# Kernel tuning notes

Hardware: AMD Instinct MI355X
Metric: run time of the kernel (lower is better)

The kernel has to match this reference:

```python
import jax, jax.numpy as jnp
import numpy as np
from jax import lax

SR = 4      # sr_ratio
HEADS = 8   # num_heads


def _upsample_bilinear_ac(x, out_h, out_w):
    # torch nn.Upsample(scale_factor=SR, mode='bilinear', align_corners=True)
    B, C, h, w = x.shape
    ys = jnp.linspace(0.0, h - 1.0, out_h)
    xs = jnp.linspace(0.0, w - 1.0, out_w)
    y0 = jnp.floor(ys).astype(jnp.int32)
    y1 = jnp.minimum(y0 + 1, h - 1)
    wy = (ys - y0).astype(x.dtype)
    x0 = jnp.floor(xs).astype(jnp.int32)
    x1 = jnp.minimum(x0 + 1, w - 1)
    wx = (xs - x0).astype(x.dtype)
    r = x[:, :, y0, :] * (1.0 - wy)[None, None, :, None] + x[:, :, y1, :] * wy[None, None, :, None]
    return r[:, :, :, x0] * (1.0 - wx) + r[:, :, :, x1] * wx


def _forward(x, sr_w, sr_b, ln_g, ln_b, q_w, k1_w, v1_w, k2_w, v2_w, proj_w, proj_b):
    B, C, H, W = x.shape
    ID = C // 4                      # internal_dim
    hd = ID // HEADS                 # head_dim
    scale = float(hd) ** -0.5
    # spatial-reduction conv for Q path: [B, ID, H/4, W/4]
    qf = lax.conv_general_dilated(x, sr_w, (SR, SR), 'VALID',
                                  dimension_numbers=('NCHW', 'OIHW', 'NCHW'))
    qf = qf + sr_b[None, :, None, None]
    Hs, Ws = qf.shape[2], qf.shape[3]
    N = Hs * Ws
    qf = qf.reshape(B, ID, N).transpose(0, 2, 1)          # [B, N, ID]
    # LayerNorm
    mu = qf.mean(-1, keepdims=True)
    var = qf.var(-1, keepdims=True)
    qn = (qf - mu) / jnp.sqrt(var + 1e-5) * ln_g + ln_b
    q = qn @ q_w                                          # [B, N, ID]
    # max / avg pooled K,V inputs: [B, N, C]
    xm = lax.reduce_window(x, -jnp.inf, lax.max, (1, 1, SR, SR), (1, 1, SR, SR), 'VALID')
    xm = xm.reshape(B, C, N).transpose(0, 2, 1)
    xa = lax.reduce_window(x, 0.0, lax.add, (1, 1, SR, SR), (1, 1, SR, SR), 'VALID') / float(SR * SR)
    xa = xa.reshape(B, C, N).transpose(0, 2, 1)

    def heads(t):
        return t.reshape(B, N, HEADS, hd).transpose(0, 2, 1, 3)  # [B, H, N, hd]

    qh = heads(q)
    k1, v1 = heads(xm @ k1_w), heads(xm @ v1_w)
    k2, v2 = heads(xa @ k2_w), heads(xa @ v2_w)

    def attend(k, v):
        a = jax.nn.softmax(jnp.einsum('bhnd,bhmd->bhnm', qh, k) * scale, axis=-1)
        return jnp.einsum('bhnm,bhmd->bhnd', a, v)

    z = attend(k1, v1) + attend(k2, v2)                   # [B, H, N, hd]
    z = z.transpose(0, 2, 1, 3).reshape(B, N, ID)
    z = z @ proj_w + proj_b                               # [B, N, C]
    z = z.transpose(0, 2, 1).reshape(B, C, Hs, Ws)
    return _upsample_bilinear_ac(z, H, W)


def setup_inputs() -> dict:
    key = jax.random.key(0)
    ks = jax.random.split(key, 9)
    B, C, H, W = 16, 256, 112, 112
    ID = C // 4

    def n(k, shape, s=0.02):
        return jax.random.normal(k, shape, jnp.float32) * s

    return {
        'x': jax.random.normal(ks[0], (B, C, H, W), jnp.float32),
        'sr_w': n(ks[1], (ID, C, SR, SR)),
        'sr_b': jnp.zeros((ID,), jnp.float32),
        'ln_g': jnp.ones((ID,), jnp.float32),
        'ln_b': jnp.zeros((ID,), jnp.float32),
        'q_w': n(ks[2], (ID, ID)),
        'k1_w': n(ks[3], (C, ID)),
        'v1_w': n(ks[4], (C, ID)),
        'k2_w': n(ks[5], (C, ID)),
        'v2_w': n(ks[6], (C, ID)),
        'proj_w': n(ks[7], (ID, C)),
        'proj_b': jnp.zeros((C,), jnp.float32),
    }


def reference(x, sr_w, sr_b, ln_g, ln_b, q_w, k1_w, v1_w, k2_w, v2_w, proj_w, proj_b):
    return _forward(x, sr_w, sr_b, ln_g, ln_b, q_w, k1_w, v1_w, k2_w, v2_w, proj_w, proj_b)
```

## Files before the change

kernel.cpp:

```cpp
#include <hip/hip_runtime.h>
#include <math.h>

typedef __attribute__((ext_vector_type(8))) short short8;
typedef __attribute__((ext_vector_type(4))) short bh4;
typedef __attribute__((ext_vector_type(4))) float f32x4;
typedef __attribute__((ext_vector_type(2))) unsigned uint2v;
typedef __attribute__((ext_vector_type(4))) unsigned uint4v;

#define MFMA16(A,B,C) __builtin_amdgcn_mfma_f32_16x16x32_bf16(A,B,C,0,0,0)

#if __has_builtin(__builtin_amdgcn_mfma_f32_16x16x16bf16_1k)
#define MFMA16x16(A,B,C) __builtin_amdgcn_mfma_f32_16x16x16bf16_1k(A,B,C,0,0,0)
#else
__device__ __forceinline__ f32x4 mfma16x16_asm(bh4 a, bh4 b, f32x4 c){
    asm volatile("v_mfma_f32_16x16x16_bf16 %0, %1, %2, %0" : "+v"(c) : "v"(a), "v"(b));
    return c;
}
#define MFMA16x16(A,B,C) mfma16x16_asm(A,B,C)
#endif

__device__ __forceinline__ unsigned short f2b(float f){
    unsigned u = __builtin_bit_cast(unsigned, f);
    return (unsigned short)((u + 0x7fffu + ((u>>16)&1u)) >> 16);
}
__device__ __forceinline__ unsigned pk2(float a, float b){
    return (unsigned)f2b(a) | ((unsigned)f2b(b) << 16);
}
__device__ __forceinline__ unsigned pk2rn(float a, float b){
    unsigned ua = __builtin_bit_cast(unsigned, a) + 0x8000u;
    unsigned ub = __builtin_bit_cast(unsigned, b) + 0x8000u;
    return (ua >> 16) | (ub & 0xffff0000u);
}


__global__ __launch_bounds__(256) void ktw(const float* __restrict__ srw,
    const float* __restrict__ qw, const float* __restrict__ k1w,
    const float* __restrict__ v1w, const float* __restrict__ k2w,
    const float* __restrict__ v2w, char* __restrict__ srwb,
    char* __restrict__ Wtm, char* __restrict__ Wta, char* __restrict__ QWt)
{
    int blk = blockIdx.x, t = threadIdx.x;
    if (blk < 128){
        int base = blk*2048 + t*8;
        float4 a = *(const float4*)(srw + base);
        float4 b = *(const float4*)(srw + base + 4);
        uint4 u = { pk2(a.x,a.y), pk2(a.z,a.w), pk2(b.x,b.y), pk2(b.z,b.w) };
        *(uint4*)(srwb + (size_t)base*2) = u;
    } else if (blk < 136){
        __shared__ float T[256*33];
        int idx = blk - 128, fi = idx >> 1, half = idx & 1;
        const float* src = (fi==0) ? k1w : (fi==1) ? v1w : (fi==2) ? k2w : v2w;
        char* dst = ((fi < 2) ? Wtm : Wta) + (size_t)((fi & 1)*64 + half*32) * 512;
        for (int li = t; li < 8192; li += 256){
            int c = li >> 5, o = li & 31;
            T[c*33 + o] = src[c*64 + half*32 + o];
        }
        __syncthreads();
        for (int lo = t; lo < 1024; lo += 256){
            int o = lo >> 5, c8 = lo & 31;
            float v[8];
            #pragma unroll
            for (int k = 0; k < 8; ++k) v[k] = T[(c8*8 + k)*33 + o];
            uint4 u = { pk2(v[0],v[1]), pk2(v[2],v[3]), pk2(v[4],v[5]), pk2(v[6],v[7]) };
            *(uint4*)(dst + o*512 + c8*16) = u;
        }
    } else {
        __shared__ float T[64*65];
        for (int li = t; li < 4096; li += 256)
            T[(li >> 6)*65 + (li & 63)] = qw[li];
        __syncthreads();
        for (int lo = t; lo < 512; lo += 256){
            int o = lo >> 3, i8 = lo & 7;
            float v[8];
            #pragma unroll
            for (int k = 0; k < 8; ++k) v[k] = T[(i8*8 + k)*65 + o];
            uint4 u = { pk2(v[0],v[1]), pk2(v[2],v[3]), pk2(v[4],v[5]), pk2(v[6],v[7]) };
            *(uint4*)(QWt + o*128 + i8*16) = u;
        }
    }
}

__global__ __launch_bounds__(256, 4) void k1(const float* __restrict__ x,
    const char* __restrict__ srwb, char* __restrict__ R, float* __restrict__ pws)
{
    __shared__ float pm[28*66];
    __shared__ float pa[28*66];
    int blk = blockIdx.x;
    int b = blk / 112, r5 = blk % 112, hs = r5 >> 2, cg4 = r5 & 3;
    int t = threadIdx.x;
    int w = t >> 6, l = t & 63, lr = l & 15, lg = l >> 4;
    int cpar = lg >> 1, r0 = (lg & 1) * 2;
    f32x4 acc0 = {0.f,0.f,0.f,0.f}, acc1 = {0.f,0.f,0.f,0.f};
    const float* xc = x + (size_t)(b*256 + cg4*64)*12544 + (size_t)(hs*4 + r0)*112;
    const char* Brow = srwb + (size_t)(w*16 + lr)*8192 + cg4*2048 + lg*16;
    int p0 = lr, p1 = min(16 + lr, 27);

    f32x4 A0,A1,A2,A3; uint4v Ba;
    f32x4 C0,C1,C2,C3; uint4v Bc;
    f32x4 D0,D1,D2,D3; uint4v Bd;
    f32x4 E0,E1,E2,E3; uint4v Be;

#define ISSUE(Xa,Xb,Xc,Xd,Bv,KS) do{ \
    const float* _s = xc + (size_t)((KS)*2 + cpar)*12544; \
    const char*  _bp = Brow + (KS)*64; \
    asm volatile("global_load_dwordx4 %0, %1, off" : "=&v"(Xa) : "v"(_s + p0*4)); \
    asm volatile("global_load_dwordx4 %0, %1, off" : "=&v"(Xb) : "v"(_s + 112 + p0*4)); \
    asm volatile("global_load_dwordx4 %0, %1, off" : "=&v"(Xc) : "v"(_s + p1*4)); \
    asm volatile("global_load_dwordx4 %0, %1, off" : "=&v"(Xd) : "v"(_s + 112 + p1*4)); \
    asm volatile("global_load_dwordx4 %0, %1, off" : "=&v"(Bv) : "v"(_bp)); }while(0)

#define WAITN(N) do{ asm volatile("s_waitcnt vmcnt(" #N ")" ::: "memory"); \
                     __builtin_amdgcn_sched_barrier(0); }while(0)

#define COMP(Xa,Xb,Xc,Xd,Bv,KS) do{ \
    if (w == 0){ \
        float mx0 = fmaxf(fmaxf(fmaxf(Xa[0],Xa[1]),fmaxf(Xa[2],Xa[3])), \
                          fmaxf(fmaxf(Xb[0],Xb[1]),fmaxf(Xb[2],Xb[3]))); \
        float sm0 = (Xa[0]+Xa[1])+(Xa[2]+Xa[3])+(Xb[0]+Xb[1])+(Xb[2]+Xb[3]); \
        float mx1 = fmaxf(fmaxf(fmaxf(Xc[0],Xc[1]),fmaxf(Xc[2],Xc[3])), \
                          fmaxf(fmaxf(Xd[0],Xd[1]),fmaxf(Xd[2],Xd[3]))); \
        float sm1 = (Xc[0]+Xc[1])+(Xc[2]+Xc[3])+(Xd[0]+Xd[1])+(Xd[2]+Xd[3]); \
        mx0 = fmaxf(mx0, __shfl_xor(mx0, 16, 64)); \
        sm0 = sm0 + __shfl_xor(sm0, 16, 64); \
        mx1 = fmaxf(mx1, __shfl_xor(mx1, 16, 64)); \
        sm1 = sm1 + __shfl_xor(sm1, 16, 64); \
        if ((lg & 1) == 0){ \
            int c = (KS)*2 + cpar; \
            pm[p0*66 + c] = mx0; pa[p0*66 + c] = sm0 * (1.f/16.f); \
            if (lr < 12){ pm[p1*66 + c] = mx1; pa[p1*66 + c] = sm1 * (1.f/16.f); } \
        } \
    } \
    short8 af0 = __builtin_bit_cast(short8, \
        (uint4v){ pk2(Xa[0],Xa[1]), pk2(Xa[2],Xa[3]), pk2(Xb[0],Xb[1]), pk2(Xb[2],Xb[3]) }); \
    short8 af1 = __builtin_bit_cast(short8, \
        (uint4v){ pk2(Xc[0],Xc[1]), pk2(Xc[2],Xc[3]), pk2(Xd[0],Xd[1]), pk2(Xd[2],Xd[3]) }); \
    short8 bf = __builtin_bit_cast(short8, Bv); \
    acc0 = MFMA16(af0, bf, acc0); \
    acc1 = MFMA16(af1, bf, acc1); }while(0)

    ISSUE(A0,A1,A2,A3,Ba, 0);
    ISSUE(C0,C1,C2,C3,Bc, 1);
    ISSUE(D0,D1,D2,D3,Bd, 2);
    ISSUE(E0,E1,E2,E3,Be, 3);
    #pragma unroll 1
    for (int it = 0; it < 7; ++it){
        int s4 = it*4;
        WAITN(15); COMP(A0,A1,A2,A3,Ba, s4+0); ISSUE(A0,A1,A2,A3,Ba, s4+4);
        WAITN(15); COMP(C0,C1,C2,C3,Bc, s4+1); ISSUE(C0,C1,C2,C3,Bc, s4+5);
        WAITN(15); COMP(D0,D1,D2,D3,Bd, s4+2); ISSUE(D0,D1,D2,D3,Bd, s4+6);
        WAITN(15); COMP(E0,E1,E2,E3,Be, s4+3); ISSUE(E0,E1,E2,E3,Be, s4+7);
    }
    WAITN(15); COMP(A0,A1,A2,A3,Ba, 28);
    WAITN(10); COMP(C0,C1,C2,C3,Bc, 29);
    WAITN(5);  COMP(D0,D1,D2,D3,Bd, 30);
    WAITN(0);  COMP(E0,E1,E2,E3,Be, 31);

#undef ISSUE
#undef WAITN
#undef COMP

    size_t rowB = (size_t)b*784 + hs*28;
    float* pp = pws + (size_t)((b*28 + hs)*4 + cg4)*1792;
    #pragma unroll
    for (int rg = 0; rg < 4; ++rg){
        int m0 = lg*4 + rg, m1 = 16 + lg*4 + rg;
        pp[m0*64 + w*16 + lr] = acc0[rg];
        if (m1 < 28) pp[m1*64 + w*16 + lr] = acc1[rg];
    }
    __syncthreads();
    if (t < 224){
        int m = t >> 3, sub = t & 7;
        float vm[8], va8[8];
        #pragma unroll
        for (int k = 0; k < 8; ++k){
            vm[k]  = pm[m*66 + sub*8 + k];
            va8[k] = pa[m*66 + sub*8 + k];
        }
        uint4 um = { pk2(vm[0],vm[1]), pk2(vm[2],vm[3]), pk2(vm[4],vm[5]), pk2(vm[6],vm[7]) };
        uint4 ua = { pk2(va8[0],va8[1]), pk2(va8[2],va8[3]), pk2(va8[4],va8[5]), pk2(va8[6],va8[7]) };
        *(uint4*)(R + (rowB + m)*1024 + cg4*128 + sub*16)       = um;
        *(uint4*)(R + (rowB + m)*1024 + 512 + cg4*128 + sub*16) = ua;
    }
}

__global__ __launch_bounds__(512) void k2(const float* __restrict__ pws_,
    const float* __restrict__ srb, const float* __restrict__ lng,
    const float* __restrict__ lnb, const char* __restrict__ Wtm,
    const char* __restrict__ Wta, const char* __restrict__ QWt,
    char* __restrict__ R)
{
    __shared__ __align__(16) char PM[16384];
    __shared__ __align__(16) char PA[16384];
    __shared__ float Db[32*64];
    __shared__ __align__(16) char QN[4096];
    int blk = blockIdx.x, b = blk/28, hs = blk%28;
    int t = threadIdx.x, w = t>>6, l = t&63, lr = l&15, lg = l>>4;
    size_t rowB = (size_t)b*784 + hs*28;
    const char* Rb = R + rowB*1024;
    for (int li = t; li < 896; li += 512){
        int m = li >> 5, c16 = li & 31;
        uint4 vm = *(const uint4*)(Rb + (size_t)m*1024 + c16*16);
        uint4 va = *(const uint4*)(Rb + (size_t)m*1024 + 512 + c16*16);
        int dst = m*512 + ((c16*16) ^ ((m&7)<<4));
        *(uint4*)(PM + dst) = vm;
        *(uint4*)(PA + dst) = va;
    }
    const float* p0 = pws_ + (size_t)(b*28 + hs)*4*1792;
    for (int e = t; e < 1792; e += 512)
        Db[e] = ((p0[e] + p0[1792+e]) + (p0[3584+e] + p0[5376+e])) + srb[e & 63];
    __syncthreads();
    float g = lng[l], be = lnb[l];
    #pragma unroll
    for (int i = 0; i < 4; ++i){
        int m = w + i*8;
        float v = Db[m*64 + l];
        float s = v, ss = v*v;
        #pragma unroll
        for (int off = 1; off < 64; off <<= 1){
            s  += __shfl_xor(s,  off, 64);
            ss += __shfl_xor(ss, off, 64);
        }
        float mu = s * (1.f/64.f);
        float var = ss * (1.f/64.f) - mu*mu;
        float qn = (v - mu) * rsqrtf(var + 1e-5f) * g + be;
        *(unsigned short*)(QN + m*128 + ((l*2) ^ ((m&7)<<4))) = f2b(qn);
    }
    __syncthreads();
    int fam = w >> 2, ofp = w & 3;
    const char* PMA = fam ? PA : PM;
    const char* Wt  = fam ? Wta : Wtm;
    f32x4 a00={0.f,0.f,0.f,0.f}, a01=a00, a10=a00, a11=a00;
    int swzr = (lr & 7) << 4;
    #pragma unroll
    for (int ks = 0; ks < 8; ++ks){
        int kb = ks*64 + lg*16;
        short8 x0 = *(const short8*)(PMA + lr*512 + (kb ^ swzr));
        short8 x1 = *(const short8*)(PMA + (16+lr)*512 + (kb ^ swzr));
        short8 b0 = *(const short8*)(Wt + (size_t)(ofp*32 + lr)*512 + kb);
        short8 b1 = *(const short8*)(Wt + (size_t)(ofp*32 + 16 + lr)*512 + kb);
        a00 = MFMA16(x0, b0, a00); a01 = MFMA16(x0, b1, a01);
        a10 = MFMA16(x1, b0, a10); a11 = MFMA16(x1, b1, a11);
    }
    f32x4 q0={0.f,0.f,0.f,0.f}, q1=q0;
    if (w < 4){
        #pragma unroll
        for (int ks = 0; ks < 2; ++ks){
            int kb = ks*64 + lg*16;
            short8 xa_ = *(const short8*)(QN + lr*128 + (kb ^ swzr));
            short8 xb_ = *(const short8*)(QN + (16+lr)*128 + (kb ^ swzr));
            short8 bq  = *(const short8*)(QWt + (size_t)(w*16 + lr)*128 + kb);
            q0 = MFMA16(xa_, bq, q0);
            q1 = MFMA16(xb_, bq, q1);
        }
    }
    #pragma unroll
    for (int j = 0; j < 2; ++j){
        int o128 = ofp*32 + j*16 + lr;
        int o = o128 & 63, hh = o >> 3, dd = o & 7, mat = fam*2 + (o128 >> 6);
        int byteoff = 128 + hh*64 + mat*16 + dd*2;
        f32x4 am  = j ? a01 : a00;
        f32x4 am1 = j ? a11 : a10;
        #pragma unroll
        for (int rg = 0; rg < 4; ++rg){
            int m0 = lg*4 + rg, m1 = 16 + lg*4 + rg;
            *(unsigned short*)(R + (rowB + m0)*1024 + byteoff) = f2b(am[rg]);
            if (m1 < 28)
                *(unsigned short*)(R + (rowB + m1)*1024 + byteoff) = f2b(am1[rg]);
        }
    }
    if (w < 4){
        int o = w*16 + lr;
        #pragma unroll
        for (int rg = 0; rg < 4; ++rg){
            int m0 = lg*4 + rg, m1 = 16 + lg*4 + rg;
            *(unsigned short*)(R + (rowB + m0)*1024 + o*2) = f2b(q0[rg]);
            if (m1 < 28)
                *(unsigned short*)(R + (rowB + m1)*1024 + o*2) = f2b(q1[rg]);
        }
    }
}

__global__ __launch_bounds__(256) void kattn(const char* __restrict__ R, float* __restrict__ z)
{
    __shared__ __align__(16) char QT [6144];
    __shared__ __align__(16) char K1b[5376];
    __shared__ __align__(16) char K2b[5376];
    __shared__ __align__(16) char VT1[3840];
    __shared__ __align__(16) char VT2[3840];
    int blk = blockIdx.x;
    int bh = blk / 7, nseg = blk % 7;
    int b = bh >> 3, h = bh & 7;
    int t = threadIdx.x, w = t >> 6, l = t & 63;
    int col = l & 15, g = l >> 4;

    for (int i = t; i < 384; i += 256) ((uint4*)QT)[i] = uint4{0,0,0,0};
    for (int i = t; i < 112; i += 256){
        *(uint4*)(K1b + i*48 + 16) = uint4{0,0,0,0};
        *(uint4*)(K2b + i*48 + 16) = uint4{0,0,0,0};
    }
    for (int i = t; i < 120; i += 256){
        *(uint4*)(VT1 + 1920 + i*16) = uint4{0,0,0,0};
        *(uint4*)(VT2 + 1920 + i*16) = uint4{0,0,0,0};
    }
    __syncthreads();
    if (t < 112){
        uint4 qv = *(const uint4*)(R + ((size_t)b*784 + nseg*112 + t)*1024 + h*16);
        *(uint2*)(QT + t*48)     = uint2{qv.x, qv.y};
        *(uint2*)(QT + t*48 + 8) = uint2{qv.z, qv.w};
    }
    __syncthreads();

    bh4 qf[2];
    #pragma unroll
    for (int nf = 0; nf < 2; ++nf)
        qf[nf] = *(const bh4*)(QT + (w*28 + nf*16 + col)*48 + g*8);

    f32x4 o1[2] = {{0,0,0,0},{0,0,0,0}}, o2[2] = {{0,0,0,0},{0,0,0,0}};
    float d1[2] = {0.f,0.f}, d2[2] = {0.f,0.f};
    const float C2 = 0.51004244f;

    for (int mt = 0; mt < 7; ++mt){
        __syncthreads();
        for (int li = t; li < 448; li += 256){
            int m = li >> 2, part = li & 3;
            uint4 v = *(const uint4*)(R + ((size_t)b*784 + mt*112 + m)*1024 + 128 + h*64 + part*16);
            if ((part & 1) == 0){
                char* Kb = (part == 0) ? K1b : K2b;
                *(uint2*)(Kb + m*48)     = uint2{v.x, v.y};
                *(uint2*)(Kb + m*48 + 8) = uint2{v.z, v.w};
            } else {
                char* Vb = (part == 1) ? VT1 : VT2;
                unsigned arr[4] = {v.x, v.y, v.z, v.w};
                #pragma unroll
                for (int d = 0; d < 4; ++d){
                    *(unsigned short*)(Vb + (d*2)*240   + m*2) = (unsigned short)(arr[d] & 0xffffu);
                    *(unsigned short*)(Vb + (d*2+1)*240 + m*2) = (unsigned short)(arr[d] >> 16);
                }
            }
        }
        __syncthreads();
        #pragma unroll
        for (int mc = 0; mc < 7; ++mc){
            bh4 ka = *(const bh4*)(K1b + (mc*16 + col)*48 + g*8);
            bh4 kb = *(const bh4*)(K2b + (mc*16 + col)*48 + g*8);
            bh4 va = *(const bh4*)(VT1 + col*240 + mc*32 + g*8);
            bh4 vb = *(const bh4*)(VT2 + col*240 + mc*32 + g*8);
            #pragma unroll
            for (int nf = 0; nf < 2; ++nf){
                f32x4 zr = {0.f,0.f,0.f,0.f};
                f32x4 s1 = MFMA16x16(ka, qf[nf], zr);
                float p0 = exp2f(s1[0]*C2), p1 = exp2f(s1[1]*C2);
                float p2 = exp2f(s1[2]*C2), p3 = exp2f(s1[3]*C2);
                d1[nf] += (p0+p1)+(p2+p3);
                bh4 pf1 = __builtin_bit_cast(bh4, (uint2v){pk2rn(p0,p1), pk2rn(p2,p3)});
                o1[nf] = MFMA16x16(va, pf1, o1[nf]);
                f32x4 s2 = MFMA16x16(kb, qf[nf], zr);
                float r0 = exp2f(s2[0]*C2), r1 = exp2f(s2[1]*C2);
                float r2 = exp2f(s2[2]*C2), r3 = exp2f(s2[3]*C2);
                d2[nf] += (r0+r1)+(r2+r3);
                bh4 pf2 = __builtin_bit_cast(bh4, (uint2v){pk2rn(r0,r1), pk2rn(r2,r3)});
                o2[nf] = MFMA16x16(vb, pf2, o2[nf]);
            }
        }
    }
    #pragma unroll
    for (int nf = 0; nf < 2; ++nf){
        d1[nf] += __shfl_xor(d1[nf], 16, 64); d1[nf] += __shfl_xor(d1[nf], 32, 64);
        d2[nf] += __shfl_xor(d2[nf], 16, 64); d2[nf] += __shfl_xor(d2[nf], 32, 64);
    }
    if (g < 2){
        #pragma unroll
        for (int nf = 0; nf < 2; ++nf){
            if (nf == 1 && col >= 12) continue;
            int n = nseg*112 + w*28 + nf*16 + col;
            float ra = 1.f / d1[nf], rb = 1.f / d2[nf];
            float4 ov;
            ov.x = o1[nf][0]*ra + o2[nf][0]*rb;
            ov.y = o1[nf][1]*ra + o2[nf][1]*rb;
            ov.z = o1[nf][2]*ra + o2[nf][2]*rb;
            ov.w = o1[nf][3]*ra + o2[nf][3]*rb;
            *(float4*)(z + ((size_t)b*784 + n)*64 + h*8 + g*4) = ov;
        }
    }
}

__global__ __launch_bounds__(256) void kpu(const float* __restrict__ z,
    const float* __restrict__ pw, const float* __restrict__ pb,
    float* __restrict__ out)
{
    __shared__ float plane[8*784];
    __shared__ float wsl[64*8];
    __shared__ int   ti0[112];
    __shared__ float twv[112];
    int blk = blockIdx.x;
    int b = blk >> 5, cg = blk & 31;
    int t = threadIdx.x;
    if (t < 128){
        #pragma unroll
        for (int q = 0; q < 4; ++q){
            int idx = t*4 + q; int o = idx >> 3, j = idx & 7;
            wsl[o*8 + j] = pw[o*256 + cg*8 + j];
        }
    }
    if (t < 112){
        float s = (float)t * (27.f/111.f);
        int i0 = (int)s; if (i0 > 27) i0 = 27;
        ti0[t] = i0; twv[t] = s - (float)i0;
    }
    __syncthreads();
    {
        int nh = t >> 1, jh = (t & 1) * 4;
        float bias0 = pb[cg*8 + jh], bias1 = pb[cg*8 + jh + 1];
        float bias2 = pb[cg*8 + jh + 2], bias3 = pb[cg*8 + jh + 3];
        for (int n = nh; n < 784; n += 128){
            const float* zr = z + ((size_t)b*784 + n)*64;
            float a0 = bias0, a1 = bias1, a2 = bias2, a3 = bias3;
            #pragma unroll
            for (int o4 = 0; o4 < 16; ++o4){
                float4 zv = *(const float4*)(zr + o4*4);
                const float* wr = wsl + (o4*4)*8 + jh;
                a0 = fmaf(zv.x, wr[0],  a0); a1 = fmaf(zv.x, wr[1],  a1);
                a2 = fmaf(zv.x, wr[2],  a2); a3 = fmaf(zv.x, wr[3],  a3);
                a0 = fmaf(zv.y, wr[8],  a0); a1 = fmaf(zv.y, wr[9],  a1);
                a2 = fmaf(zv.y, wr[10], a2); a3 = fmaf(zv.y, wr[11], a3);
                a0 = fmaf(zv.z, wr[16], a0); a1 = fmaf(zv.z, wr[17], a1);
                a2 = fmaf(zv.z, wr[18], a2); a3 = fmaf(zv.z, wr[19], a3);
                a0 = fmaf(zv.w, wr[24], a0); a1 = fmaf(zv.w, wr[25], a1);
                a2 = fmaf(zv.w, wr[26], a2); a3 = fmaf(zv.w, wr[27], a3);
            }
            plane[(jh+0)*784 + n] = a0;
            plane[(jh+1)*784 + n] = a1;
            plane[(jh+2)*784 + n] = a2;
            plane[(jh+3)*784 + n] = a3;
        }
    }
    __syncthreads();
    float* ob = out + ((size_t)b*256 + cg*8)*12544;
    for (int i = t; i < 12544; i += 256){
        int y = i/112, xx = i%112;
        int y0 = ti0[y], x0 = ti0[xx];
        float wy = twv[y], wx = twv[xx];
        int y1 = min(y0+1, 27), x1 = min(x0+1, 27);
        int i00 = y0*28 + x0, i01 = y0*28 + x1, i10 = y1*28 + x0, i11 = y1*28 + x1;
        #pragma unroll
        for (int j = 0; j < 8; ++j){
            const float* pl = plane + j*784;
            float a  = pl[i00] + (pl[i10]-pl[i00])*wy;
            float bb = pl[i01] + (pl[i11]-pl[i01])*wy;
            ob[(size_t)j*12544 + i] = a + (bb-a)*wx;
        }
    }
}

extern "C" void kernel_launch(void* const* d_in, const int* in_sizes, int n_in,
                              void* d_out, int out_size, void* d_ws, size_t ws_size,
                              hipStream_t stream) {
    const float* x   = (const float*)d_in[0];
    const float* srw = (const float*)d_in[1];
    const float* srb = (const float*)d_in[2];
    const float* lng = (const float*)d_in[3];
    const float* lnb = (const float*)d_in[4];
    const float* qw  = (const float*)d_in[5];
    const float* k1w = (const float*)d_in[6];
    const float* v1w = (const float*)d_in[7];
    const float* k2w = (const float*)d_in[8];
    const float* v2w = (const float*)d_in[9];
    const float* pw  = (const float*)d_in[10];
    const float* pb  = (const float*)d_in[11];

    char*  Rws  = (char*)d_ws;
    float* pws  = (float*)(Rws + 12845056);
    char*  srwb = Rws + 25690112;
    char*  Wtm  = Rws + 26214400;
    char*  Wta  = Rws + 26279936;
    char*  QWt  = Rws + 26345472;
    float* z    = (float*)(Rws + 12845056);
    float* out  = (float*)d_out;

    ktw  <<<137,  256, 0, stream>>>(srw, qw, k1w, v1w, k2w, v2w, srwb, Wtm, Wta, QWt);
    k1   <<<1792, 256, 0, stream>>>(x, srwb, Rws, pws);
    k2   <<<448,  512, 0, stream>>>(pws, srb, lng, lnb, Wtm, Wta, QWt, Rws);
    kattn<<<896,  256, 0, stream>>>(Rws, z);
    kpu  <<<512,  256, 0, stream>>>(z, pw, pb, out);
}
```

Baseline: 270.6 us.

## Split conv reduction across two wave groups and vectorize upsample stores

The spatial-reduction conv kernel now runs 512 threads per block. Two groups of four waves each handle half of the channel reduction, and each group writes its own partial-sum slab, so the workspace doubles and later buffers move to new offsets. The LayerNorm kernel sums eight partials instead of four. The bilinear upsample in the final kernel now computes four adjacent output pixels per thread and writes them as one float4 store. The aim is to shorten the serial load/MFMA chain per wave and cut store instruction count, at the price of more partial-sum traffic and different occupancy.

Result: no change. 267.2 us (-1.3%).

```diff
diff --git a/kernel.cpp b/kernel.cpp
--- a/kernel.cpp
+++ b/kernel.cpp
@@ -80,7 +80,7 @@
     }
 }
 
-__global__ __launch_bounds__(256, 4) void k1(const float* __restrict__ x,
+__global__ __launch_bounds__(512, 3) void k1(const float* __restrict__ x,
     const char* __restrict__ srwb, char* __restrict__ R, float* __restrict__ pws)
 {
     __shared__ float pm[28*66];
@@ -89,11 +89,14 @@
     int b = blk / 112, r5 = blk % 112, hs = r5 >> 2, cg4 = r5 & 3;
     int t = threadIdx.x;
     int w = t >> 6, l = t & 63, lr = l & 15, lg = l >> 4;
+    int ofr = w & 3, kh = w >> 2;
+    int ks0 = kh*16;
     int cpar = lg >> 1, r0 = (lg & 1) * 2;
     f32x4 acc0 = {0.f,0.f,0.f,0.f}, acc1 = {0.f,0.f,0.f,0.f};
     const float* xc = x + (size_t)(b*256 + cg4*64)*12544 + (size_t)(hs*4 + r0)*112;
-    const char* Brow = srwb + (size_t)(w*16 + lr)*8192 + cg4*2048 + lg*16;
+    const char* Brow = srwb + (size_t)(ofr*16 + lr)*8192 + cg4*2048 + lg*16;
     int p0 = lr, p1 = min(16 + lr, 27);
+    bool poolw = (ofr == 0);
 
     f32x4 A0,A1,A2,A3; uint4v Ba;
     f32x4 C0,C1,C2,C3; uint4v Bc;
@@ -113,7 +116,7 @@
                      __builtin_amdgcn_sched_barrier(0); }while(0)
 
 #define COMP(Xa,Xb,Xc,Xd,Bv,KS) do{ \
-    if (w == 0){ \
+    if (poolw){ \
         float mx0 = fmaxf(fmaxf(fmaxf(Xa[0],Xa[1]),fmaxf(Xa[2],Xa[3])), \
                           fmaxf(fmaxf(Xb[0],Xb[1]),fmaxf(Xb[2],Xb[3]))); \
         float sm0 = (Xa[0]+Xa[1])+(Xa[2]+Xa[3])+(Xb[0]+Xb[1])+(Xb[2]+Xb[3]); \
@@ -138,34 +141,34 @@
     acc0 = MFMA16(af0, bf, acc0); \
     acc1 = MFMA16(af1, bf, acc1); }while(0)
 
-    ISSUE(A0,A1,A2,A3,Ba, 0);
-    ISSUE(C0,C1,C2,C3,Bc, 1);
-    ISSUE(D0,D1,D2,D3,Bd, 2);
-    ISSUE(E0,E1,E2,E3,Be, 3);
+    ISSUE(A0,A1,A2,A3,Ba, ks0+0);
+    ISSUE(C0,C1,C2,C3,Bc, ks0+1);
+    ISSUE(D0,D1,D2,D3,Bd, ks0+2);
+    ISSUE(E0,E1,E2,E3,Be, ks0+3);
     #pragma unroll 1
-    for (int it = 0; it < 7; ++it){
-        int s4 = it*4;
+    for (int it = 0; it < 3; ++it){
+        int s4 = ks0 + it*4;
         WAITN(15); COMP(A0,A1,A2,A3,Ba, s4+0); ISSUE(A0,A1,A2,A3,Ba, s4+4);
         WAITN(15); COMP(C0,C1,C2,C3,Bc, s4+1); ISSUE(C0,C1,C2,C3,Bc, s4+5);
         WAITN(15); COMP(D0,D1,D2,D3,Bd, s4+2); ISSUE(D0,D1,D2,D3,Bd, s4+6);
         WAITN(15); COMP(E0,E1,E2,E3,Be, s4+3); ISSUE(E0,E1,E2,E3,Be, s4+7);
     }
-    WAITN(15); COMP(A0,A1,A2,A3,Ba, 28);
-    WAITN(10); COMP(C0,C1,C2,C3,Bc, 29);
-    WAITN(5);  COMP(D0,D1,D2,D3,Bd, 30);
-    WAITN(0);  COMP(E0,E1,E2,E3,Be, 31);
+    WAITN(15); COMP(A0,A1,A2,A3,Ba, ks0+12);
+    WAITN(10); COMP(C0,C1,C2,C3,Bc, ks0+13);
+    WAITN(5);  COMP(D0,D1,D2,D3,Bd, ks0+14);
+    WAITN(0);  COMP(E0,E1,E2,E3,Be, ks0+15);
 
 #undef ISSUE
 #undef WAITN
 #undef COMP
 
     size_t rowB = (size_t)b*784 + hs*28;
-    float* pp = pws + (size_t)((b*28 + hs)*4 + cg4)*1792;
+    float* pp = pws + (size_t)(((b*28 + hs)*4 + cg4)*2 + kh)*1792;
     #pragma unroll
     for (int rg = 0; rg < 4; ++rg){
         int m0 = lg*4 + rg, m1 = 16 + lg*4 + rg;
-        pp[m0*64 + w*16 + lr] = acc0[rg];
-        if (m1 < 28) pp[m1*64 + w*16 + lr] = acc1[rg];
+        pp[m0*64 + ofr*16 + lr] = acc0[rg];
+        if (m1 < 28) pp[m1*64 + ofr*16 + lr] = acc1[rg];
     }
     __syncthreads();
     if (t < 224){
@@ -205,9 +208,10 @@
         *(uint4*)(PM + dst) = vm;
         *(uint4*)(PA + dst) = va;
     }
-    const float* p0 = pws_ + (size_t)(b*28 + hs)*4*1792;
+    const float* p0 = pws_ + (size_t)(b*28 + hs)*8*1792;
     for (int e = t; e < 1792; e += 512)
-        Db[e] = ((p0[e] + p0[1792+e]) + (p0[3584+e] + p0[5376+e])) + srb[e & 63];
+        Db[e] = (((p0[e] + p0[1792+e]) + (p0[3584+e] + p0[5376+e]))
+              + ((p0[7168+e] + p0[8960+e]) + (p0[10752+e] + p0[12544+e]))) + srb[e & 63];
     __syncthreads();
     float g = lng[l], be = lnb[l];
     #pragma unroll
@@ -436,18 +440,31 @@
     }
     __syncthreads();
     float* ob = out + ((size_t)b*256 + cg*8)*12544;
-    for (int i = t; i < 12544; i += 256){
-        int y = i/112, xx = i%112;
-        int y0 = ti0[y], x0 = ti0[xx];
-        float wy = twv[y], wx = twv[xx];
-        int y1 = min(y0+1, 27), x1 = min(x0+1, 27);
-        int i00 = y0*28 + x0, i01 = y0*28 + x1, i10 = y1*28 + x0, i11 = y1*28 + x1;
+    for (int i4 = t; i4 < 3136; i4 += 256){
+        int y = i4 / 28, xq = (i4 % 28) * 4;
+        int y0 = ti0[y], y1 = min(y0+1, 27);
+        float wy = twv[y];
+        int x0q[4], x1q[4]; float wxq[4];
+        #pragma unroll
+        for (int qi = 0; qi < 4; ++qi){
+            int xx = xq + qi;
+            x0q[qi] = ti0[xx]; x1q[qi] = min(x0q[qi]+1, 27); wxq[qi] = twv[xx];
+        }
+        int base = y*112 + xq;
         #pragma unroll
         for (int j = 0; j < 8; ++j){
-            const float* pl = plane + j*784;
-            float a  = pl[i00] + (pl[i10]-pl[i00])*wy;
-            float bb = pl[i01] + (pl[i11]-pl[i01])*wy;
-            ob[(size_t)j*12544 + i] = a + (bb-a)*wx;
+            const float* r0p = plane + j*784 + y0*28;
+            const float* r1p = plane + j*784 + y1*28;
+            float4 ov;
+            #pragma unroll
+            for (int qi = 0; qi < 4; ++qi){
+                float a  = r0p[x0q[qi]] + (r1p[x0q[qi]] - r0p[x0q[qi]])*wy;
+                float bb = r0p[x1q[qi]] + (r1p[x1q[qi]] - r0p[x1q[qi]])*wy;
+                float v = a + (bb - a)*wxq[qi];
+                if (qi == 0) ov.x = v; else if (qi == 1) ov.y = v;
+                else if (qi == 2) ov.z = v; else ov.w = v;
+            }
+            *(float4*)(ob + (size_t)j*12544 + base) = ov;
         }
     }
 }
@@ -470,15 +487,15 @@
 
     char*  Rws  = (char*)d_ws;
     float* pws  = (float*)(Rws + 12845056);
-    char*  srwb = Rws + 25690112;
-    char*  Wtm  = Rws + 26214400;
-    char*  Wta  = Rws + 26279936;
-    char*  QWt  = Rws + 26345472;
+    char*  srwb = Rws + 38535168;
+    char*  Wtm  = Rws + 39059456;
+    char*  Wta  = Rws + 39124992;
+    char*  QWt  = Rws + 39190528;
     float* z    = (float*)(Rws + 12845056);
     float* out  = (float*)d_out;
 
     ktw  <<<137,  256, 0, stream>>>(srw, qw, k1w, v1w, k2w, v2w, srwb, Wtm, Wta, QWt);
-    k1   <<<1792, 256, 0, stream>>>(x, srwb, Rws, pws);
+    k1   <<<1792, 512, 0, stream>>>(x, srwb, Rws, pws);
     k2   <<<448,  512, 0, stream>>>(pws, srb, lng, lnb, Wtm, Wta, QWt, Rws);
     kattn<<<896,  256, 0, stream>>>(Rws, z);
     kpu  <<<512,  256, 0, stream>>>(z, pw, pb, out);
```
